# Performance work log

Measured on AMD Instinct MI355X. Metric: run time of the kernel, lower is better.

Reference implementation:

```python
import jax, jax.numpy as jnp
import numpy as np

EPS = 1e-05

# NOTE on faithfulness: in the original forward, all make_groups_tensor (BFP
# quantization) results for sum/avg/var are OVERWRITTEN by exact recomputation
# (`avg = y.view(C,-1).mean(-1); var = y.view(C,-1).var(-1, unbiased=False)`),
# and with bfp_conf.fo=False the output is not quantized either. Hence the
# effective forward math is exact training-mode BatchNorm2d:
#   out = (x - mean_bchw) * rsqrt(var_bchw + eps) * gamma + beta

def setup_inputs() -> dict:
    key = jax.random.key(0)
    k1, k2 = jax.random.split(key)
    B, C, H, W = 64, 256, 56, 56
    x = jax.random.normal(k1, (B, C, H, W), dtype=jnp.float32)
    gamma = jax.random.uniform(k2, (C,), dtype=jnp.float32)  # reset_parameters: uniform_()
    beta = jnp.zeros((C,), dtype=jnp.float32)
    return {"x": x, "gamma": gamma, "beta": beta}


def reference(x, gamma, beta):
    # per-channel stats over (B, H, W), biased variance
    mean = jnp.mean(x, axis=(0, 2, 3), keepdims=True)            # [1,C,1,1]
    var = jnp.mean((x - mean) ** 2, axis=(0, 2, 3), keepdims=True)
    scale = jax.lax.rsqrt(var + EPS)
    out = (x - mean) * scale
    return out * gamma.reshape(1, -1, 1, 1) + beta.reshape(1, -1, 1, 1)
```

## Files before the change

kernel.cpp:

```cpp
#include <hip/hip_runtime.h>


#define EPS 1e-5f
constexpr int B_ = 64;
constexpr int C_ = 256;
constexpr int HW_ = 56 * 56;
constexpr int HW4_ = HW_ / 4;
constexpr int NPC_ = B_ * HW_;
constexpr unsigned int TOTAL4_ = (unsigned int)B_ * C_ * HW4_;

__global__ void __launch_bounds__(256) bn_partial(const float* __restrict__ x,
                                                  float* __restrict__ psum,
                                                  float* __restrict__ psumsq) {
    const int plane = blockIdx.x;
    const float4* xp = (const float4*)(x + (size_t)plane * HW_);

    float s = 0.f, ss = 0.f;
    for (int i = threadIdx.x; i < HW4_; i += 256) {
        float4 v = xp[i];
        s  += v.x + v.y + v.z + v.w;
        ss += v.x * v.x + v.y * v.y + v.z * v.z + v.w * v.w;
    }

    for (int off = 32; off > 0; off >>= 1) {
        s  += __shfl_down(s, off);
        ss += __shfl_down(ss, off);
    }
    __shared__ float ls[8];
    const int wave = threadIdx.x >> 6;
    const int lane = threadIdx.x & 63;
    if (lane == 0) { ls[wave] = s; ls[4 + wave] = ss; }
    __syncthreads();
    if (threadIdx.x == 0) {
        float S  = ls[0] + ls[1] + ls[2] + ls[3];
        float SS = ls[4] + ls[5] + ls[6] + ls[7];
        const int b = plane / C_;
        const int c = plane % C_;
        psum[c * B_ + b]   = S;
        psumsq[c * B_ + b] = SS;
    }
}

__global__ void __launch_bounds__(64) bn_finalize(const float* __restrict__ psum,
                                                  const float* __restrict__ psumsq,
                                                  const float* __restrict__ gamma,
                                                  const float* __restrict__ beta,
                                                  float* __restrict__ scale,
                                                  float* __restrict__ shift) {
    const int c = blockIdx.x;
    const int t = threadIdx.x;
    float s  = psum[c * B_ + t];
    float ss = psumsq[c * B_ + t];
    for (int off = 32; off > 0; off >>= 1) {
        s  += __shfl_down(s, off);
        ss += __shfl_down(ss, off);
    }
    if (t == 0) {
        const float invN = 1.0f / (float)NPC_;
        float mean = s * invN;
        float var  = ss * invN - mean * mean;
        float sc   = gamma[c] * rsqrtf(var + EPS);
        scale[c] = sc;
        shift[c] = beta[c] - mean * sc;
    }
}

__global__ void __launch_bounds__(256) bn_apply(const float* __restrict__ x,
                                                const float* __restrict__ scale,
                                                const float* __restrict__ shift,
                                                float* __restrict__ out) {
    const unsigned int i = blockIdx.x * 256u + threadIdx.x;
    if (i >= TOTAL4_) return;
    const int c = (int)((i / (unsigned int)HW4_) % (unsigned int)C_);
    float4 v = ((const float4*)x)[i];
    const float sc = scale[c];
    const float sh = shift[c];
    float4 o;
    o.x = v.x * sc + sh;
    o.y = v.y * sc + sh;
    o.z = v.z * sc + sh;
    o.w = v.w * sc + sh;
    ((float4*)out)[i] = o;
}

extern "C" void kernel_launch(void* const* d_in, const int* in_sizes, int n_in,
                              void* d_out, int out_size, void* d_ws, size_t ws_size,
                              hipStream_t stream) {
    const float* x     = (const float*)d_in[0];
    const float* gamma = (const float*)d_in[1];
    const float* beta  = (const float*)d_in[2];
    float* out = (float*)d_out;

    float* psum   = (float*)d_ws;
    float* psumsq = psum + B_ * C_;
    float* scale  = psumsq + B_ * C_;
    float* shift  = scale + C_;

    bn_partial<<<B_ * C_, 256, 0, stream>>>(x, psum, psumsq);
    bn_finalize<<<C_, 64, 0, stream>>>(psum, psumsq, gamma, beta, scale, shift);
    const unsigned int nblk = (TOTAL4_ + 255u) / 256u;
    bn_apply<<<nblk, 256, 0, stream>>>(x, scale, shift, out);
}
```

Measured before the change: 371.7 us.

## Batch stats blocks over multiple planes, nontemporal output stores, simpler finalize

The stats kernel now has each block accumulate 8 batch planes for one channel, so the grid shrinks from 16384 to 2048 blocks and per-block reduction overhead drops. The finalize kernel becomes one thread per channel summing 8 partials instead of a wave shuffle over 64. The apply kernel drops its bounds check, replaces the modulo with a mask, and writes output with nontemporal stores to avoid polluting cache. The tradeoff is fewer blocks and less parallelism in the stats pass, plus longer serial accumulation per thread.

```diff
diff --git a/kernel.cpp b/kernel.cpp
--- a/kernel.cpp
+++ b/kernel.cpp
@@ -7,19 +7,27 @@
 constexpr int HW_ = 56 * 56;
 constexpr int HW4_ = HW_ / 4;
 constexpr int NPC_ = B_ * HW_;
+constexpr int PB_ = 8;
+constexpr int NB_ = B_ / PB_;
 constexpr unsigned int TOTAL4_ = (unsigned int)B_ * C_ * HW4_;
 
-__global__ void __launch_bounds__(256) bn_partial(const float* __restrict__ x,
-                                                  float* __restrict__ psum,
-                                                  float* __restrict__ psumsq) {
-    const int plane = blockIdx.x;
-    const float4* xp = (const float4*)(x + (size_t)plane * HW_);
+typedef float vfloat4 __attribute__((ext_vector_type(4)));
+
+__global__ void __launch_bounds__(256) bn_stats(const float* __restrict__ x,
+                                                float* __restrict__ psum,
+                                                float* __restrict__ psumsq) {
+    const int c  = blockIdx.x & (C_ - 1);
+    const int bg = blockIdx.x >> 8;
 
     float s = 0.f, ss = 0.f;
-    for (int i = threadIdx.x; i < HW4_; i += 256) {
-        float4 v = xp[i];
-        s  += v.x + v.y + v.z + v.w;
-        ss += v.x * v.x + v.y * v.y + v.z * v.z + v.w * v.w;
+    for (int p = 0; p < PB_; ++p) {
+        const int plane = (bg * PB_ + p) * C_ + c;
+        const vfloat4* xp = (const vfloat4*)(x + (size_t)plane * HW_);
+        for (int i = threadIdx.x; i < HW4_; i += 256) {
+            vfloat4 v = xp[i];
+            s  += v.x + v.y + v.z + v.w;
+            ss += v.x * v.x + v.y * v.y + v.z * v.z + v.w * v.w;
+        }
     }
 
     for (int off = 32; off > 0; off >>= 1) {
@@ -32,12 +40,8 @@
     if (lane == 0) { ls[wave] = s; ls[4 + wave] = ss; }
     __syncthreads();
     if (threadIdx.x == 0) {
-        float S  = ls[0] + ls[1] + ls[2] + ls[3];
-        float SS = ls[4] + ls[5] + ls[6] + ls[7];
-        const int b = plane / C_;
-        const int c = plane % C_;
-        psum[c * B_ + b]   = S;
-        psumsq[c * B_ + b] = SS;
+        psum[c * NB_ + bg]   = ls[0] + ls[1] + ls[2] + ls[3];
+        psumsq[c * NB_ + bg] = ls[4] + ls[5] + ls[6] + ls[7];
     }
 }
 
@@ -47,22 +51,18 @@
                                                   const float* __restrict__ beta,
                                                   float* __restrict__ scale,
                                                   float* __restrict__ shift) {
-    const int c = blockIdx.x;
-    const int t = threadIdx.x;
-    float s  = psum[c * B_ + t];
-    float ss = psumsq[c * B_ + t];
-    for (int off = 32; off > 0; off >>= 1) {
-        s  += __shfl_down(s, off);
-        ss += __shfl_down(ss, off);
+    const int c = blockIdx.x * 64 + threadIdx.x;
+    float s = 0.f, ss = 0.f;
+    for (int j = 0; j < NB_; ++j) {
+        s  += psum[c * NB_ + j];
+        ss += psumsq[c * NB_ + j];
     }
-    if (t == 0) {
-        const float invN = 1.0f / (float)NPC_;
-        float mean = s * invN;
-        float var  = ss * invN - mean * mean;
-        float sc   = gamma[c] * rsqrtf(var + EPS);
-        scale[c] = sc;
-        shift[c] = beta[c] - mean * sc;
-    }
+    const float invN = 1.0f / (float)NPC_;
+    const float mean = s * invN;
+    const float var  = ss * invN - mean * mean;
+    const float sc   = gamma[c] * rsqrtf(var + EPS);
+    scale[c] = sc;
+    shift[c] = beta[c] - mean * sc;
 }
 
 __global__ void __launch_bounds__(256) bn_apply(const float* __restrict__ x,
@@ -70,17 +70,16 @@
                                                 const float* __restrict__ shift,
                                                 float* __restrict__ out) {
     const unsigned int i = blockIdx.x * 256u + threadIdx.x;
-    if (i >= TOTAL4_) return;
-    const int c = (int)((i / (unsigned int)HW4_) % (unsigned int)C_);
-    float4 v = ((const float4*)x)[i];
+    const unsigned int c = (i / (unsigned int)HW4_) & (C_ - 1u);
+    vfloat4 v = ((const vfloat4*)x)[i];
     const float sc = scale[c];
     const float sh = shift[c];
-    float4 o;
+    vfloat4 o;
     o.x = v.x * sc + sh;
     o.y = v.y * sc + sh;
     o.z = v.z * sc + sh;
     o.w = v.w * sc + sh;
-    ((float4*)out)[i] = o;
+    __builtin_nontemporal_store(o, (vfloat4*)out + i);
 }
 
 extern "C" void kernel_launch(void* const* d_in, const int* in_sizes, int n_in,
@@ -92,12 +91,11 @@
     float* out = (float*)d_out;
 
     float* psum   = (float*)d_ws;
-    float* psumsq = psum + B_ * C_;
-    float* scale  = psumsq + B_ * C_;
+    float* psumsq = psum + C_ * NB_;
+    float* scale  = psumsq + C_ * NB_;
     float* shift  = scale + C_;
 
-    bn_partial<<<B_ * C_, 256, 0, stream>>>(x, psum, psumsq);
-    bn_finalize<<<C_, 64, 0, stream>>>(psum, psumsq, gamma, beta, scale, shift);
-    const unsigned int nblk = (TOTAL4_ + 255u) / 256u;
-    bn_apply<<<nblk, 256, 0, stream>>>(x, scale, shift, out);
+    bn_stats<<<C_ * NB_, 256, 0, stream>>>(x, psum, psumsq);
+    bn_finalize<<<C_ / 64, 64, 0, stream>>>(psum, psumsq, gamma, beta, scale, shift);
+    bn_apply<<<TOTAL4_ / 256u, 256, 0, stream>>>(x, scale, shift, out);
 }
```

Result: no change. 371.9 us (+0.1%).
